# Performance work log

Measured on AMD Instinct MI355X. Metric: run time of the kernel, lower is better.

The kernel has to match this reference:

```python
import jax, jax.numpy as jnp
import numpy as np

B, C, H = 16, 512, 8
T_PI, T_P = 2048, 512  # mel frames, text tokens


def setup_inputs() -> dict:
    key = jax.random.key(0)
    ks = jax.random.split(key, 8)
    pi = jax.random.uniform(ks[0], (B, T_PI), dtype=jnp.float32) * T_P  # mel positions in text coords
    p = jax.random.uniform(ks[1], (B, T_P), dtype=jnp.float32) * T_P   # text positions
    x_h = jax.random.normal(ks[2], (B, C, T_P), dtype=jnp.float32)
    text_mask = jnp.ones((B, T_P), dtype=bool)
    sigma = jnp.ones((H,), dtype=jnp.float32) * 0.1
    w_hidden = jax.random.normal(ks[3], (2 * C, C), dtype=jnp.float32) / np.sqrt(C)
    b_hidden = jnp.zeros((2 * C,), dtype=jnp.float32)
    w_out = jax.random.normal(ks[4], (C, 2 * C), dtype=jnp.float32) / np.sqrt(2 * C)
    b_out = jnp.zeros((C,), dtype=jnp.float32)
    return {"pi": pi, "p": p, "x_h": x_h, "text_mask": text_mask,
            "sigma": sigma, "w_hidden": w_hidden, "b_hidden": b_hidden,
            "w_out": w_out, "b_out": b_out}


def reference(pi, p, x_h, text_mask, sigma, w_hidden, b_hidden, w_out, b_out):
    # Gaussian position-distance energies: (B, T_pi, T_p)
    energies = -(pi[:, :, None] - p[:, None, :]) ** 2
    real_sigma = jnp.clip(sigma, 1e-6, 3.0)  # (H,)
    # scale per head -> (B, H, T_pi, T_p)
    energies = energies[:, None, :, :] * real_sigma[None, :, None, None]
    energies = jnp.where(text_mask[:, None, None, :], energies, -jnp.inf)
    attns = jax.nn.softmax(energies, axis=-1)  # (B, H, T_pi, T_p)

    # 1x1 conv C -> 2C: h (B, 2C, T_p)
    h = jnp.einsum('oc,bct->bot', w_hidden, x_h) + b_hidden[None, :, None]
    Bh, twoC, Tp = h.shape
    nH = real_sigma.shape[0]
    d = twoC // nH
    h = h.reshape(Bh, nH, d, Tp).transpose(0, 1, 3, 2)  # (B, H, T_p, d)

    out = jnp.einsum('bhqt,bhtd->bhqd', attns, h)        # (B, H, T_pi, d)
    out = out.transpose(0, 1, 3, 2).reshape(Bh, twoC, -1)  # (B, 2C, T_pi)
    out = jnp.einsum('oc,bct->bot', w_out, out) + b_out[None, :, None]  # (B, C, T_pi)
    return (out, attns, real_sigma)
```

## Files before the change

kernel.cpp:

```cpp
#include <hip/hip_runtime.h>
#include <stdint.h>


typedef float  f32x4  __attribute__((ext_vector_type(4)));
typedef short  bf16x8 __attribute__((ext_vector_type(8)));

namespace {
constexpr int Bn = 16, Cc = 512, Hh = 8, TQ = 2048, TP = 512, Dd = 128, C2 = 1024;
constexpr size_t ATT_OFF = (size_t)Bn * Cc * TQ;
constexpr size_t SIG_OFF = ATT_OFF + (size_t)Bn * Hh * TQ * TP;
constexpr size_t XT_ELEMS  = (size_t)Bn * TP * Cc;
constexpr size_t WHB_ELEMS = (size_t)C2 * Cc;
constexpr size_t WOB_ELEMS = (size_t)Cc * C2;
constexpr size_t HWS_ELEMS = (size_t)Bn * Hh * Dd * TP;
constexpr size_t YWS_ELEMS = (size_t)Bn * TQ * C2;
}

__device__ inline ushort f2bf(float f) {
    uint32_t u = __float_as_uint(f);
    u += 0x7FFFu + ((u >> 16) & 1u);
    return (ushort)(u >> 16);
}

__device__ inline void gload16(const ushort* g, ushort* l) {
    __builtin_amdgcn_global_load_lds(
        (const __attribute__((address_space(1))) uint32_t*)g,
        (__attribute__((address_space(3))) uint32_t*)l, 16, 0, 0);
}

__global__ __launch_bounds__(256) void k_prep(
    const float* __restrict__ wh, const float* __restrict__ wo,
    const float* __restrict__ sg,
    ushort* __restrict__ whb, ushort* __restrict__ wob, float* __restrict__ sigo)
{
    int i = blockIdx.x * 256 + threadIdx.x;
    float4 a = *reinterpret_cast<const float4*>(&wh[(size_t)i * 4]);
    float4 b = *reinterpret_cast<const float4*>(&wo[(size_t)i * 4]);
    ushort4 ua, ub;
    ua.x = f2bf(a.x); ua.y = f2bf(a.y); ua.z = f2bf(a.z); ua.w = f2bf(a.w);
    ub.x = f2bf(b.x); ub.y = f2bf(b.y); ub.z = f2bf(b.z); ub.w = f2bf(b.w);
    *reinterpret_cast<ushort4*>(&whb[(size_t)i * 4]) = ua;
    *reinterpret_cast<ushort4*>(&wob[(size_t)i * 4]) = ub;
    if (i < Hh) sigo[i] = fminf(fmaxf(sg[i], 1e-6f), 3.0f);
}

__global__ __launch_bounds__(256) void k_xt(
    const float* __restrict__ x, ushort* __restrict__ xT)
{
    __shared__ float tile[64 * 67];
    int bid = blockIdx.x;
    int tt = bid & 7, cb = (bid >> 3) & 7, b = bid >> 6;
    int c0 = cb * 64, t0 = tt * 64;
    int tid = threadIdx.x;
    #pragma unroll
    for (int it = 0; it < 4; ++it) {
        int idx = it * 256 + tid;
        int rc = idx >> 4, tc = (idx & 15) * 4;
        float4 v = *reinterpret_cast<const float4*>(
            &x[((size_t)b * Cc + c0 + rc) * TP + t0 + tc]);
        tile[rc * 67 + tc + 0] = v.x; tile[rc * 67 + tc + 1] = v.y;
        tile[rc * 67 + tc + 2] = v.z; tile[rc * 67 + tc + 3] = v.w;
    }
    __syncthreads();
    #pragma unroll
    for (int it = 0; it < 4; ++it) {
        int idx = it * 256 + tid;
        int rt = idx >> 4, cc = (idx & 15) * 4;
        ushort4 o;
        o.x = f2bf(tile[(cc + 0) * 67 + rt]);
        o.y = f2bf(tile[(cc + 1) * 67 + rt]);
        o.z = f2bf(tile[(cc + 2) * 67 + rt]);
        o.w = f2bf(tile[(cc + 3) * 67 + rt]);
        *reinterpret_cast<ushort4*>(&xT[((size_t)b * TP + t0 + rt) * Cc + c0 + cc]) = o;
    }
}

__global__ __launch_bounds__(256) void k_hidden(
    const ushort* __restrict__ xT,
    const ushort* __restrict__ whb,
    const float*  __restrict__ bias,
    ushort* __restrict__ hws)
{
    __shared__ __align__(16) ushort As[128 * 64];
    __shared__ __align__(16) ushort Bs[128 * 64];
    __shared__ float bias_s[128];

    int bid = blockIdx.x;
    int no = bid & 7, mq = (bid >> 3) & 3, b = bid >> 5;
    int t0 = mq * 128, o0 = no * 128;
    int tid = threadIdx.x, l = tid & 63, w = tid >> 6;
    int wm = (w >> 1) * 64, wn = (w & 1) * 64;
    int r = l & 15, g = l >> 4;
    if (tid < 128) bias_s[tid] = bias[o0 + tid];

    int srow = (l >> 3);
    int sch  = l & 7;

    f32x4 acc[4][4];
    #pragma unroll
    for (int m = 0; m < 4; ++m)
        #pragma unroll
        for (int n = 0; n < 4; ++n) acc[m][n] = (f32x4){0.f, 0.f, 0.f, 0.f};

    const ushort* agbase = xT + ((size_t)b * TP + t0) * Cc;
    const ushort* bgbase = whb + (size_t)o0 * Cc;

    for (int k0 = 0; k0 < Cc; k0 += 64) {
        __syncthreads();
        #pragma unroll
        for (int it = 0; it < 4; ++it) {
            int c = w + it * 4;
            int row = c * 8 + srow;
            int chs = sch ^ (row & 7);
            gload16(&agbase[(size_t)row * Cc + k0 + chs * 8], &As[c * 512]);
            gload16(&bgbase[(size_t)row * Cc + k0 + chs * 8], &Bs[c * 512]);
        }
        __syncthreads();
        #pragma unroll
        for (int s = 0; s < 2; ++s) {
            bf16x8 av[4], bv[4];
            #pragma unroll
            for (int m = 0; m < 4; ++m) {
                int row = wm + m * 16 + r;
                av[m] = *reinterpret_cast<const bf16x8*>(
                    &As[row * 64 + (((s * 4 + g) ^ (row & 7)) * 8)]);
            }
            #pragma unroll
            for (int n = 0; n < 4; ++n) {
                int row = wn + n * 16 + r;
                bv[n] = *reinterpret_cast<const bf16x8*>(
                    &Bs[row * 64 + (((s * 4 + g) ^ (row & 7)) * 8)]);
            }
            #pragma unroll
            for (int m = 0; m < 4; ++m)
                #pragma unroll
                for (int n = 0; n < 4; ++n)
                    acc[m][n] = __builtin_amdgcn_mfma_f32_16x16x32_bf16(
                        av[m], bv[n], acc[m][n], 0, 0, 0);
        }
    }
    #pragma unroll
    for (int n = 0; n < 4; ++n) {
        int ol = wn + n * 16 + r;
        int og = o0 + ol;
        float bi = bias_s[ol];
        int hh = og >> 7, d = og & 127;
        #pragma unroll
        for (int m = 0; m < 4; ++m) {
            int t = t0 + wm + m * 16 + g * 4;
            ushort4 v;
            v.x = f2bf(acc[m][n][0] + bi); v.y = f2bf(acc[m][n][1] + bi);
            v.z = f2bf(acc[m][n][2] + bi); v.w = f2bf(acc[m][n][3] + bi);
            *reinterpret_cast<ushort4*>(&hws[(((size_t)b * Hh + hh) * Dd + d) * TP + t]) = v;
        }
    }
}

__global__ __launch_bounds__(256) void k_attw(
    const float* __restrict__ pi, const float* __restrict__ p,
    const float* __restrict__ sgm,
    float* __restrict__ attns, float2* __restrict__ nrm)
{
    __shared__ __align__(16) float p_s[TP];
    __shared__ float pim_s[64];

    int bid = blockIdx.x;
    int qt = bid & 31, hh = (bid >> 5) & 7, b = bid >> 8;
    int q0 = qt * 64;
    int tid = threadIdx.x, l = tid & 63, w = tid >> 6;
    float sig = fminf(fmaxf(sgm[hh], 1e-6f), 3.0f), nsig = -sig;

    for (int i = tid; i < TP; i += 256) p_s[i] = p[(size_t)b * TP + i];
    if (tid < 64) pim_s[tid] = pi[(size_t)b * TQ + q0 + tid];
    __syncthreads();

    float* abase = attns + (((size_t)b * Hh + hh) * TQ + q0) * TP;
    float2* nbase = nrm + ((size_t)b * Hh + hh) * TQ + q0;

    for (int rr = 0; rr < 16; ++rr) {
        int qloc = w * 16 + rr;
        float piq = pim_s[qloc];
        float d2[8];
        #pragma unroll
        for (int i = 0; i < 8; ++i) { float df = piq - p_s[l + 64 * i]; d2[i] = df * df; }
        float dmin = d2[0];
        #pragma unroll
        for (int i = 1; i < 8; ++i) dmin = fminf(dmin, d2[i]);
        #pragma unroll
        for (int off = 32; off; off >>= 1) dmin = fminf(dmin, __shfl_xor(dmin, off));
        float negm = sig * dmin;
        float vv[8], ssum = 0.f;
        #pragma unroll
        for (int i = 0; i < 8; ++i) { vv[i] = __expf(fmaf(d2[i], nsig, negm)); ssum += vv[i]; }
        #pragma unroll
        for (int off = 32; off; off >>= 1) ssum += __shfl_xor(ssum, off);
        float inv = 1.0f / ssum;
        if (l == 0) nbase[qloc] = make_float2(negm, inv);
        float* aptr = abase + (size_t)qloc * TP + l;
        #pragma unroll
        for (int i = 0; i < 8; ++i)
            __builtin_nontemporal_store(vv[i] * inv, &aptr[64 * i]);
    }
}

__global__ __launch_bounds__(256) void k_pv(
    const float* __restrict__ pi, const float* __restrict__ p,
    const float* __restrict__ sgm, const ushort* __restrict__ hws,
    const float2* __restrict__ nrm, ushort* __restrict__ y)
{
    __shared__ __align__(16) float  p_s[TP];
    __shared__ float pim_s[64];
    __shared__ float negm_s[64];
    __shared__ float inv_s[64];
    __shared__ __align__(16) ushort Ht0[128 * 64];
    __shared__ __align__(16) ushort Ht1[128 * 64];
    __shared__ __align__(16) ushort yst_all[4][16 * 132];

    int bid = blockIdx.x;
    int qt = bid & 31, hh = (bid >> 5) & 7, b = bid >> 8;
    int q0 = qt * 64;
    int tid = threadIdx.x, l = tid & 63, w = tid >> 6;
    float sig = fminf(fmaxf(sgm[hh], 1e-6f), 3.0f), nsig = -sig;

    const ushort* hb = hws + (size_t)(b * Hh + hh) * Dd * TP;
    int srow = l >> 3, sch = l & 7;

    #pragma unroll
    for (int it = 0; it < 4; ++it) {
        int c = w + it * 4;
        int row = c * 8 + srow;
        int chs = sch ^ (row & 7);
        gload16(&hb[(size_t)row * TP + chs * 8], &Ht0[c * 512]);
    }
    for (int i = tid; i < TP; i += 256) p_s[i] = p[(size_t)b * TP + i];
    if (tid < 64) {
        pim_s[tid] = pi[(size_t)b * TQ + q0 + tid];
        float2 nv = nrm[((size_t)b * Hh + hh) * TQ + q0 + tid];
        negm_s[tid] = nv.x; inv_s[tid] = nv.y;
    }
    __syncthreads();

    int r = l & 15, g = l >> 4;
    int qloc = w * 16 + r;
    float piq = pim_s[qloc], negm = negm_s[qloc];
    f32x4 acc[8];
    #pragma unroll
    for (int n = 0; n < 8; ++n) acc[n] = (f32x4){0.f, 0.f, 0.f, 0.f};

    ushort* curb = Ht0;
    ushort* nxtb = Ht1;

    for (int tt = 0; tt < TP; tt += 64) {
        if (tt + 64 < TP) {
            #pragma unroll
            for (int it = 0; it < 4; ++it) {
                int c = w + it * 4;
                int row = c * 8 + srow;
                int chs = sch ^ (row & 7);
                gload16(&hb[(size_t)row * TP + tt + 64 + chs * 8], &nxtb[c * 512]);
            }
        }
        #pragma unroll
        for (int s = 0; s < 2; ++s) {
            int tb = tt + s * 32 + g * 8;
            float4 pv0 = *reinterpret_cast<const float4*>(&p_s[tb]);
            float4 pv1 = *reinterpret_cast<const float4*>(&p_s[tb + 4]);
            float pvv[8] = {pv0.x, pv0.y, pv0.z, pv0.w, pv1.x, pv1.y, pv1.z, pv1.w};
            bf16x8 af;
            #pragma unroll
            for (int j = 0; j < 8; ++j) {
                float df = piq - pvv[j];
                af[j] = (short)f2bf(__expf(fmaf(df * df, nsig, negm)));
            }
            #pragma unroll
            for (int n = 0; n < 8; ++n) {
                int row = n * 16 + r;
                bf16x8 bv = *reinterpret_cast<const bf16x8*>(
                    &curb[row * 64 + (((s * 4 + g) ^ (row & 7)) * 8)]);
                acc[n] = __builtin_amdgcn_mfma_f32_16x16x32_bf16(af, bv, acc[n], 0, 0, 0);
            }
        }
        __syncthreads();
        ushort* t2 = curb; curb = nxtb; nxtb = t2;
    }

    float inv4[4];
    #pragma unroll
    for (int j = 0; j < 4; ++j) inv4[j] = inv_s[w * 16 + g * 4 + j];
    ushort* yst = yst_all[w];
    #pragma unroll
    for (int n = 0; n < 8; ++n)
        #pragma unroll
        for (int j = 0; j < 4; ++j)
            yst[(g * 4 + j) * 132 + n * 16 + r] = f2bf(acc[n][j] * inv4[j]);
    __syncthreads();
    size_t ybase = (size_t)b * TQ + q0 + w * 16;
    #pragma unroll
    for (int it = 0; it < 4; ++it) {
        int idx = it * 64 + l;
        int qr = idx >> 4, c8 = (idx & 15) * 8;
        *reinterpret_cast<bf16x8*>(&y[(ybase + qr) * C2 + hh * Dd + c8]) =
            *reinterpret_cast<const bf16x8*>(&yst[qr * 132 + c8]);
    }
}

__global__ __launch_bounds__(256) void k_out(
    const ushort* __restrict__ y,
    const ushort* __restrict__ wob,
    const float*  __restrict__ bout,
    float* __restrict__ outp)
{
    __shared__ __align__(16) ushort As[128 * 64];
    __shared__ __align__(16) ushort Bs[128 * 64];
    __shared__ float bo_s[128];

    int bid = blockIdx.x;
    int no = bid & 3, mq = (bid >> 2) & 15, b = bid >> 6;
    int q0 = mq * 128, o0 = no * 128;
    int tid = threadIdx.x, l = tid & 63, w = tid >> 6;
    int wm = (w >> 1) * 64, wn = (w & 1) * 64;
    int r = l & 15, g = l >> 4;
    if (tid < 128) bo_s[tid] = bout[o0 + tid];

    int srow = (l >> 3);
    int sch  = l & 7;

    f32x4 acc[4][4];
    #pragma unroll
    for (int m = 0; m < 4; ++m)
        #pragma unroll
        for (int n = 0; n < 4; ++n) acc[m][n] = (f32x4){0.f, 0.f, 0.f, 0.f};

    const ushort* agbase = y + ((size_t)b * TQ + q0) * C2;
    const ushort* bgbase = wob + (size_t)o0 * C2;

    for (int k0 = 0; k0 < C2; k0 += 64) {
        __syncthreads();
        #pragma unroll
        for (int it = 0; it < 4; ++it) {
            int c = w + it * 4;
            int row = c * 8 + srow;
            int chs = sch ^ (row & 7);
            gload16(&agbase[(size_t)row * C2 + k0 + chs * 8], &As[c * 512]);
            gload16(&bgbase[(size_t)row * C2 + k0 + chs * 8], &Bs[c * 512]);
        }
        __syncthreads();
        #pragma unroll
        for (int s = 0; s < 2; ++s) {
            bf16x8 av[4], bv[4];
            #pragma unroll
            for (int m = 0; m < 4; ++m) {
                int row = wm + m * 16 + r;
                av[m] = *reinterpret_cast<const bf16x8*>(
                    &As[row * 64 + (((s * 4 + g) ^ (row & 7)) * 8)]);
            }
            #pragma unroll
            for (int n = 0; n < 4; ++n) {
                int row = wn + n * 16 + r;
                bv[n] = *reinterpret_cast<const bf16x8*>(
                    &Bs[row * 64 + (((s * 4 + g) ^ (row & 7)) * 8)]);
            }
            #pragma unroll
            for (int m = 0; m < 4; ++m)
                #pragma unroll
                for (int n = 0; n < 4; ++n)
                    acc[m][n] = __builtin_amdgcn_mfma_f32_16x16x32_bf16(
                        av[m], bv[n], acc[m][n], 0, 0, 0);
        }
    }
    #pragma unroll
    for (int n = 0; n < 4; ++n) {
        int ol = wn + n * 16 + r;
        float bo = bo_s[ol];
        size_t obase = ((size_t)b * Cc + o0 + ol) * TQ + q0 + wm;
        #pragma unroll
        for (int m = 0; m < 4; ++m) {
            float4 v = make_float4(acc[m][n][0] + bo, acc[m][n][1] + bo,
                                   acc[m][n][2] + bo, acc[m][n][3] + bo);
            *reinterpret_cast<float4*>(&outp[obase + m * 16 + g * 4]) = v;
        }
    }
}

extern "C" void kernel_launch(void* const* d_in, const int* in_sizes, int n_in,
                              void* d_out, int out_size, void* d_ws, size_t ws_size,
                              hipStream_t stream) {
    const float* pi    = (const float*)d_in[0];
    const float* p     = (const float*)d_in[1];
    const float* x_h   = (const float*)d_in[2];
    const float* sigma = (const float*)d_in[4];
    const float* w_h   = (const float*)d_in[5];
    const float* b_h   = (const float*)d_in[6];
    const float* w_o   = (const float*)d_in[7];
    const float* b_o   = (const float*)d_in[8];

    float* outp  = (float*)d_out;
    float* attns = outp + ATT_OFF;
    float* sigo  = outp + SIG_OFF;

    ushort* xT  = (ushort*)d_ws;
    ushort* whb = xT + XT_ELEMS;
    ushort* wob = whb + WHB_ELEMS;
    ushort* hws = wob + WOB_ELEMS;
    ushort* yws = hws + HWS_ELEMS;
    float2* nrm = (float2*)(yws + YWS_ELEMS);

    k_prep  <<<512,  256, 0, stream>>>(w_h, w_o, sigma, whb, wob, sigo);
    k_xt    <<<1024, 256, 0, stream>>>(x_h, xT);
    k_hidden<<<512,  256, 0, stream>>>(xT, whb, b_h, hws);
    k_attw  <<<4096, 256, 0, stream>>>(pi, p, sigma, attns, nrm);
    k_pv    <<<4096, 256, 0, stream>>>(pi, p, sigma, hws, nrm, yws);
    k_out   <<<1024, 256, 0, stream>>>(yws, wob, b_o, outp);
}
```

Before: 259.5 us.

## Merge hidden-projection GEMM into attention-weight kernel via interleaved block roles

Fuses the hidden 1x1-conv GEMM and the attention-weight/softmax kernel into one launch. Blocks are interleaved so every third block does a smaller 64x64 GEMM tile and the others compute attention rows. Both roles share one LDS pool. This lets the compute-bound GEMM overlap the store-bound attention writes and removes one launch boundary. The GEMM tiles shrink (less reuse per block), the async LDS load helper is replaced by plain register-staged copies, and LDS use per block grows for the attention role.

Measured after the change: 234.2 us. 1.11x faster.

```diff
diff --git a/kernel.cpp b/kernel.cpp
--- a/kernel.cpp
+++ b/kernel.cpp
@@ -75,99 +75,84 @@
     }
 }
 
-__global__ __launch_bounds__(256) void k_hidden(
+__global__ __launch_bounds__(256) void k_hattw(
     const ushort* __restrict__ xT,
     const ushort* __restrict__ whb,
     const float*  __restrict__ bias,
-    ushort* __restrict__ hws)
-{
-    __shared__ __align__(16) ushort As[128 * 64];
-    __shared__ __align__(16) ushort Bs[128 * 64];
-    __shared__ float bias_s[128];
-
-    int bid = blockIdx.x;
-    int no = bid & 7, mq = (bid >> 3) & 3, b = bid >> 5;
-    int t0 = mq * 128, o0 = no * 128;
-    int tid = threadIdx.x, l = tid & 63, w = tid >> 6;
-    int wm = (w >> 1) * 64, wn = (w & 1) * 64;
-    int r = l & 15, g = l >> 4;
-    if (tid < 128) bias_s[tid] = bias[o0 + tid];
-
-    int srow = (l >> 3);
-    int sch  = l & 7;
-
-    f32x4 acc[4][4];
-    #pragma unroll
-    for (int m = 0; m < 4; ++m)
-        #pragma unroll
-        for (int n = 0; n < 4; ++n) acc[m][n] = (f32x4){0.f, 0.f, 0.f, 0.f};
-
-    const ushort* agbase = xT + ((size_t)b * TP + t0) * Cc;
-    const ushort* bgbase = whb + (size_t)o0 * Cc;
-
-    for (int k0 = 0; k0 < Cc; k0 += 64) {
-        __syncthreads();
-        #pragma unroll
-        for (int it = 0; it < 4; ++it) {
-            int c = w + it * 4;
-            int row = c * 8 + srow;
-            int chs = sch ^ (row & 7);
-            gload16(&agbase[(size_t)row * Cc + k0 + chs * 8], &As[c * 512]);
-            gload16(&bgbase[(size_t)row * Cc + k0 + chs * 8], &Bs[c * 512]);
-        }
-        __syncthreads();
-        #pragma unroll
-        for (int s = 0; s < 2; ++s) {
-            bf16x8 av[4], bv[4];
-            #pragma unroll
-            for (int m = 0; m < 4; ++m) {
-                int row = wm + m * 16 + r;
-                av[m] = *reinterpret_cast<const bf16x8*>(
-                    &As[row * 64 + (((s * 4 + g) ^ (row & 7)) * 8)]);
-            }
-            #pragma unroll
-            for (int n = 0; n < 4; ++n) {
-                int row = wn + n * 16 + r;
-                bv[n] = *reinterpret_cast<const bf16x8*>(
-                    &Bs[row * 64 + (((s * 4 + g) ^ (row & 7)) * 8)]);
-            }
-            #pragma unroll
-            for (int m = 0; m < 4; ++m)
-                #pragma unroll
-                for (int n = 0; n < 4; ++n)
-                    acc[m][n] = __builtin_amdgcn_mfma_f32_16x16x32_bf16(
-                        av[m], bv[n], acc[m][n], 0, 0, 0);
-        }
-    }
-    #pragma unroll
-    for (int n = 0; n < 4; ++n) {
-        int ol = wn + n * 16 + r;
-        int og = o0 + ol;
-        float bi = bias_s[ol];
-        int hh = og >> 7, d = og & 127;
-        #pragma unroll
-        for (int m = 0; m < 4; ++m) {
-            int t = t0 + wm + m * 16 + g * 4;
-            ushort4 v;
-            v.x = f2bf(acc[m][n][0] + bi); v.y = f2bf(acc[m][n][1] + bi);
-            v.z = f2bf(acc[m][n][2] + bi); v.w = f2bf(acc[m][n][3] + bi);
-            *reinterpret_cast<ushort4*>(&hws[(((size_t)b * Hh + hh) * Dd + d) * TP + t]) = v;
-        }
-    }
-}
-
-__global__ __launch_bounds__(256) void k_attw(
     const float* __restrict__ pi, const float* __restrict__ p,
     const float* __restrict__ sgm,
-    float* __restrict__ attns, float2* __restrict__ nrm)
-{
-    __shared__ __align__(16) float p_s[TP];
-    __shared__ float pim_s[64];
-
+    ushort* __restrict__ hws, float* __restrict__ attns, float2* __restrict__ nrm)
+{
+    __shared__ __align__(16) ushort pool[8320];
     int bid = blockIdx.x;
-    int qt = bid & 31, hh = (bid >> 5) & 7, b = bid >> 8;
+    int tid = threadIdx.x, l = tid & 63, w = tid >> 6;
+    int tri = bid / 3, rem = bid - tri * 3;
+
+    if (rem == 0) {
+        int hid = tri;
+        int ot = hid & 15, tt = (hid >> 4) & 7, b = hid >> 7;
+        int o0 = ot * 64, t0 = tt * 64;
+        ushort* As = pool;
+        ushort* Bs = pool + 4096;
+        float* bias_s = reinterpret_cast<float*>(pool + 8192);
+        if (tid < 64) bias_s[tid] = bias[o0 + tid];
+
+        int wn = w * 16;
+        int r = l & 15, g = l >> 4;
+        f32x4 acc[4];
+        #pragma unroll
+        for (int m = 0; m < 4; ++m) acc[m] = (f32x4){0.f, 0.f, 0.f, 0.f};
+
+        const ushort* ag = xT + ((size_t)b * TP + t0) * Cc;
+        const ushort* bg = whb + (size_t)o0 * Cc;
+
+        for (int k0 = 0; k0 < Cc; k0 += 64) {
+            __syncthreads();
+            #pragma unroll
+            for (int it = 0; it < 2; ++it) {
+                int idx = it * 256 + tid;
+                int row = idx >> 3, ch = idx & 7;
+                int dst = row * 64 + ((ch ^ (row & 7)) * 8);
+                *reinterpret_cast<bf16x8*>(&As[dst]) =
+                    *reinterpret_cast<const bf16x8*>(&ag[(size_t)row * Cc + k0 + ch * 8]);
+                *reinterpret_cast<bf16x8*>(&Bs[dst]) =
+                    *reinterpret_cast<const bf16x8*>(&bg[(size_t)row * Cc + k0 + ch * 8]);
+            }
+            __syncthreads();
+            #pragma unroll
+            for (int s = 0; s < 2; ++s) {
+                int brow = wn + r;
+                bf16x8 bv = *reinterpret_cast<const bf16x8*>(
+                    &Bs[brow * 64 + (((s * 4 + g) ^ (brow & 7)) * 8)]);
+                #pragma unroll
+                for (int m = 0; m < 4; ++m) {
+                    int row = m * 16 + r;
+                    bf16x8 av = *reinterpret_cast<const bf16x8*>(
+                        &As[row * 64 + (((s * 4 + g) ^ (row & 7)) * 8)]);
+                    acc[m] = __builtin_amdgcn_mfma_f32_16x16x32_bf16(av, bv, acc[m], 0, 0, 0);
+                }
+            }
+        }
+        int og = o0 + wn + r;
+        int hh = og >> 7, d = og & 127;
+        float bi = bias_s[wn + r];
+        #pragma unroll
+        for (int m = 0; m < 4; ++m) {
+            int t = t0 + m * 16 + g * 4;
+            ushort4 v;
+            v.x = f2bf(acc[m][0] + bi); v.y = f2bf(acc[m][1] + bi);
+            v.z = f2bf(acc[m][2] + bi); v.w = f2bf(acc[m][3] + bi);
+            *reinterpret_cast<ushort4*>(&hws[(((size_t)b * Hh + hh) * Dd + d) * TP + t]) = v;
+        }
+        return;
+    }
+
+    int sub = tri * 2 + rem - 1;
+    float* p_s   = reinterpret_cast<float*>(pool);
+    float* pim_s = reinterpret_cast<float*>(pool) + 512;
+
+    int qt = sub & 31, hh = (sub >> 5) & 7, b = sub >> 8;
     int q0 = qt * 64;
-    int tid = threadIdx.x, l = tid & 63, w = tid >> 6;
     float sig = fminf(fmaxf(sgm[hh], 1e-6f), 3.0f), nsig = -sig;
 
     for (int i = tid; i < TP; i += 256) p_s[i] = p[(size_t)b * TP + i];
@@ -407,8 +392,7 @@
 
     k_prep  <<<512,  256, 0, stream>>>(w_h, w_o, sigma, whb, wob, sigo);
     k_xt    <<<1024, 256, 0, stream>>>(x_h, xT);
-    k_hidden<<<512,  256, 0, stream>>>(xT, whb, b_h, hws);
-    k_attw  <<<4096, 256, 0, stream>>>(pi, p, sigma, attns, nrm);
+    k_hattw <<<6144, 256, 0, stream>>>(xT, whb, b_h, pi, p, sigma, hws, attns, nrm);
     k_pv    <<<4096, 256, 0, stream>>>(pi, p, sigma, hws, nrm, yws);
     k_out   <<<1024, 256, 0, stream>>>(yws, wob, b_o, outp);
 }
```
